# Optimization experiments

Measured on AMD Instinct MI355X. Metric: run time of the kernel, lower is better.

## Reference

```python
import jax, jax.numpy as jnp
import numpy as np

B, L, D, H, E, M, P = 2, 512, 768, 12, 32, 4, 256
EMB, BS, MAP, C = 768, 64, 256, 97


def setup_inputs() -> dict:
    key = jax.random.key(0)
    ks = jax.random.split(key, 16)
    w = lambda k, s: (0.02 * jax.random.normal(k, s, jnp.float32))
    seq = jax.random.normal(ks[0], (B, L, D), jnp.float32)
    attn = jax.random.uniform(ks[1], (B, H, L, L), jnp.float32)
    entity_pos = jax.random.randint(ks[2], (B, E, M), 0, L - 2)
    # distinct (h, t) entity pairs per document -> unique mention-pair scatter slots
    grid = jnp.stack(jnp.meshgrid(jnp.arange(E), jnp.arange(E), indexing='ij'), -1).reshape(-1, 2)
    hts = jnp.stack([grid[jax.random.permutation(jax.random.fold_in(ks[3], b), E * E)[:P]] for b in range(B)], 0)
    mention_idx = jnp.broadcast_to(jnp.arange(E * M).reshape(E, M), (B, E, M))
    return {
        'seq': seq, 'attn': attn,
        'entity_pos': entity_pos, 'hts': hts, 'mention_idx': mention_idx,
        'W_head': w(ks[4], (2 * D, EMB)), 'b_head': jnp.zeros((EMB,), jnp.float32),
        'W_tail': w(ks[5], (2 * D, EMB)), 'b_tail': jnp.zeros((EMB,), jnp.float32),
        'W_rel': w(ks[6], (EMB * BS, C)), 'b_rel': jnp.zeros((C,), jnp.float32),
        'W_fh': w(ks[7], (D, EMB)), 'W_ft': w(ks[8], (D, EMB)), 'b_f': jnp.zeros((EMB,), jnp.float32),
        'W_unet': w(ks[9], (EMB, C)), 'b_unet': jnp.zeros((C,), jnp.float32),
        'W_mlp': w(ks[10], (EMB, C)), 'b_mlp': jnp.zeros((C,), jnp.float32),
        'W_bil': w(ks[11], (3 * C, C)), 'b_bil': jnp.zeros((C,), jnp.float32),
    }


def reference(seq, attn, entity_pos, hts, mention_idx,
              W_head, b_head, W_tail, b_tail, W_rel, b_rel,
              W_fh, W_ft, b_f, W_unet, b_unet, W_mlp, b_mlp, W_bil, b_bil):
    pos = entity_pos + 1                                 # bert offset
    b3 = jnp.arange(B)[:, None, None]
    ment_emb = seq[b3, pos]                              # [B,E,M,D] mention gather
    ment_att = attn[b3, :, pos]                          # [B,E,M,H,L]
    ent_emb = jax.nn.logsumexp(ment_emb, axis=2)         # [B,E,D] logsumexp pool
    ent_att = ment_att.mean(axis=2)                      # [B,E,H,L]
    b2 = jnp.arange(B)[:, None]
    h_idx, t_idx = hts[..., 0], hts[..., 1]
    hs, ts = ent_emb[b2, h_idx], ent_emb[b2, t_idx]      # [B,P,D]
    ha, ta = ent_att[b2, h_idx], ent_att[b2, t_idx]      # [B,P,H,L]
    ht_att = (ha * ta).mean(2)                           # [B,P,L]
    ht_att = ht_att / (ht_att.sum(-1, keepdims=True) + 1e-5)
    rs = jnp.einsum('bld,bpl->bpd', seq, ht_att)         # localized context
    N = B * P
    hz = jnp.tanh(jnp.concatenate([hs, rs], -1).reshape(N, 2 * D) @ W_head + b_head)
    tz = jnp.tanh(jnp.concatenate([ts, rs], -1).reshape(N, 2 * D) @ W_tail + b_tail)
    bl = (hz.reshape(N, EMB // BS, BS, 1) * tz.reshape(N, EMB // BS, 1, BS)).reshape(N, EMB * BS)
    r1 = bl @ W_rel + b_rel                              # [N,C]
    # mention-pair dense map scatter (map_rss)
    ment_flat = ment_emb.reshape(B, E * M, D)
    mh = mention_idx[b2, h_idx]                          # [B,P,M]
    mt = mention_idx[b2, t_idx]
    mh2 = jnp.broadcast_to(mh[:, :, :, None], (B, P, M, M))
    mt2 = jnp.broadcast_to(mt[:, :, None, :], (B, P, M, M))
    b4 = jnp.broadcast_to(jnp.arange(B)[:, None, None, None], (B, P, M, M))
    eh = ment_flat[b4, mh2]                              # [B,P,M,M,D]
    et = ment_flat[b4, mt2]
    feat = eh @ W_fh + et @ W_ft + b_f                   # fused Linear(cat(h,t))
    mp = jnp.zeros((B, MAP, MAP, EMB), seq.dtype).at[b4, mh2, mt2].set(feat)
    enc2 = jnp.tanh(mp @ W_unet + b_unet)                # UNet-channel surrogate
    enc3 = jax.nn.gelu(mp @ W_mlp + b_mlp)               # MLP-channel surrogate
    r2 = jax.nn.logsumexp(enc2[b4, mh2, mt2], axis=(2, 3)).reshape(N, C)
    r3 = jax.nn.logsumexp(enc3[b4, mh2, mt2], axis=(2, 3)).reshape(N, C)
    return jnp.concatenate([r1, r2, r3], -1) @ W_bil + b_bil
```

## Files before the change

kernel.cpp:

```cpp
#include <hip/hip_runtime.h>
#include <hip/hip_bf16.h>

#define B_  2
#define L_  512
#define D_  768
#define H_  12
#define E_  32
#define M_  4
#define P_  256
#define EMB_ 768
#define BS_ 64
#define C_  97
#define N_  (B_*P_)

#define KTOT_    49152
#define CPAD_    112
#define KSPLIT_  48
#define KCHUNK_  (KTOT_/KSPLIT_)
#define PSTR_    128
#define TILE_    (CPAD_*64)

typedef __hip_bfloat16 bf16;
typedef __attribute__((ext_vector_type(8))) short bf16x8;
typedef __attribute__((ext_vector_type(4))) float f32x4;
typedef __attribute__((ext_vector_type(8))) float f32x8;

__device__ inline float ldIn(const void* p, long idx, int isbf) {
    return isbf ? (float)((const bf16*)p)[idx] : ((const float*)p)[idx];
}

__device__ inline unsigned short f2bf(float f) {
    bf16 h = (bf16)f;
    return *(unsigned short*)&h;
}

__device__ inline int detect_bf(const void* seqd) {
    const unsigned short* u = (const unsigned short*)seqd;
    int lane = threadIdx.x & 63;
    unsigned short e = (u[lane] >> 7) & 0xFF;
    unsigned long long m = __ballot(e >= 140);
    return m == 0ull;
}

struct PrepArgs {
    const void* src[8];
    long off[8];
    int K[8];
    int Ncols[8];
    int Npad[8];
    unsigned short* dst[8];
    const void* W_bil;  float* W_bilF;
    const void* b_f; const void* W_unet; const void* b_unet;
    const void* W_mlp; const void* b_mlp; float* c23p;
    const void* W_rel; unsigned short* WBt;
    const void* seqd;
};

union PrepSm {
    float T[32][65];
    unsigned short TW[CPAD_][72];
};

__global__ void prep_kernel(PrepArgs a) {
    int isbf = detect_bf(a.seqd);
    int z = blockIdx.z;
    __shared__ PrepSm sm;
    int tid = threadIdx.x;
    if (z == 0) {
        int lin = blockIdx.y*48 + blockIdx.x;
        if (lin >= 16) return;
        int c = tid;
        if (c >= C_) return;
        float s2 = 0.f, s3 = 0.f;
        int d0 = lin*48;
        for (int i = 0; i < 48; i++) {
            int d = d0 + i;
            float bf = ldIn(a.b_f, d, isbf);
            s2 += bf * ldIn(a.W_unet, (long)d*C_ + c, isbf);
            s3 += bf * ldIn(a.W_mlp,  (long)d*C_ + c, isbf);
        }
        if (lin == 0) {
            s2 += ldIn(a.b_unet, c, isbf);
            s3 += ldIn(a.b_mlp,  c, isbf);
        }
        a.c23p[lin*194 + c]      = s2;
        a.c23p[lin*194 + 97 + c] = s3;
    } else if (z == 1) {
        int lin = blockIdx.y*48 + blockIdx.x;
        if (lin >= KTOT_/64) return;
        int k0 = lin * 64;
        for (int idx = tid; idx < 64*97; idx += 256) {
            int kk = idx / 97, c = idx % 97;
            sm.TW[c][kk] = f2bf(ldIn(a.W_rel, (long)(k0+kk)*C_ + c, isbf));
        }
        for (int idx = tid; idx < 15*64; idx += 256) {
            sm.TW[97 + (idx>>6)][idx & 63] = 0;
        }
        __syncthreads();
        unsigned short* tb = a.WBt + (long)lin*TILE_;
        for (int t = 0; t < 4; t++) {
            int idx = tid + t*256;
            if (idx < 896) {
                int l  = idx & 63;
                int h  = (idx >> 6) & 1;
                int ct = idx >> 7;
                int row = ct*16 + (l & 15);
                int col = h*32 + (l >> 4)*8;
                *(uint4*)(tb + idx*8) = *(uint4*)&sm.TW[row][col];
            }
        }
    } else if (z <= 9) {
        int j = z - 2;
        int K = a.K[j], Ncols = a.Ncols[j], Npad = a.Npad[j];
        int k0 = blockIdx.x*32, n0 = blockIdx.y*64;
        if (k0 >= K || n0 >= Npad) return;
        const void* src = a.src[j];
        long off = a.off[j];
        unsigned short* dst = a.dst[j];
        int r = tid >> 3, c8 = (tid & 7) * 8;
        if ((Ncols & 7) == 0) {
            long base = off + (long)(k0+r)*Ncols + n0 + c8;
            if (isbf) {
                unsigned short tmp[8];
                *(uint4*)tmp = *(const uint4*)((const unsigned short*)src + base);
                #pragma unroll
                for (int e = 0; e < 8; e++) {
                    bf16 hh = *(bf16*)&tmp[e];
                    sm.T[r][c8+e] = (float)hh;
                }
            } else {
                const float* sp = (const float*)src + base;
                float4 x = *(const float4*)sp;
                float4 y = *(const float4*)(sp + 4);
                sm.T[r][c8+0]=x.x; sm.T[r][c8+1]=x.y; sm.T[r][c8+2]=x.z; sm.T[r][c8+3]=x.w;
                sm.T[r][c8+4]=y.x; sm.T[r][c8+5]=y.y; sm.T[r][c8+6]=y.z; sm.T[r][c8+7]=y.w;
            }
        } else {
            #pragma unroll
            for (int e = 0; e < 8; e++) {
                int n = n0 + c8 + e;
                sm.T[r][c8+e] = (n < Ncols) ? ldIn(src, off + (long)(k0+r)*Ncols + n, isbf) : 0.f;
            }
        }
        __syncthreads();
        int nn = tid >> 2, q8 = (tid & 3) * 8;
        unsigned short o[8];
        #pragma unroll
        for (int e = 0; e < 8; e++) o[e] = f2bf(sm.T[q8+e][nn]);
        *(uint4*)(dst + (long)(n0+nn)*K + k0 + q8) = *(uint4*)o;
    } else {
        int lin = blockIdx.y*48 + blockIdx.x;
        int idx = lin*256 + tid;
        if (idx < 291*C_) a.W_bilF[idx] = ldIn(a.W_bil, idx, isbf);
    }
}

__global__ void ghatt_kernel(const void* __restrict__ seq, const void* __restrict__ attn,
                             const int* __restrict__ entity_pos, const int* __restrict__ hts,
                             unsigned short* __restrict__ mentb, float* __restrict__ ent_emb,
                             unsigned short* __restrict__ htb) {
    int isbf = detect_bf(seq);
    if (blockIdx.x < 512) {
        int bp = blockIdx.x;
        int b = bp >> 8;
        int h_e = hts[bp*2+0], t_e = hts[bp*2+1];
        int ph[M_], pt[M_];
        for (int m = 0; m < M_; m++) {
            ph[m] = entity_pos[(b*E_ + h_e)*M_ + m] + 1;
            pt[m] = entity_pos[(b*E_ + t_e)*M_ + m] + 1;
        }
        __shared__ float red[256];
        float v[2];
        for (int t = 0; t < 2; t++) {
            int l = threadIdx.x + t*256;
            float s = 0.f;
            for (int h = 0; h < H_; h++) {
                long hb = ((long)(b*H_ + h))*L_;
                float ha = 0.f, ta = 0.f;
                for (int m = 0; m < M_; m++) {
                    ha += ldIn(attn, (hb + ph[m])*L_ + l, isbf);
                    ta += ldIn(attn, (hb + pt[m])*L_ + l, isbf);
                }
                s += ha * ta;
            }
            v[t] = s * (0.0625f / H_);
        }
        red[threadIdx.x] = v[0] + v[1];
        __syncthreads();
        for (int off = 128; off > 0; off >>= 1) {
            if (threadIdx.x < off) red[threadIdx.x] += red[threadIdx.x+off];
            __syncthreads();
        }
        float inv = 1.0f / (red[0] + 1e-5f);
        for (int t = 0; t < 2; t++) {
            int l = threadIdx.x + t*256;
            htb[(long)bp*L_ + l] = f2bf(v[t] * inv);
        }
    } else {
        int be = blockIdx.x - 512;
        int b = be >> 5;
        int pos[M_];
        for (int m = 0; m < M_; m++) pos[m] = entity_pos[be*M_+m] + 1;
        for (int d = threadIdx.x; d < D_; d += 256) {
            float x[M_];
            for (int m = 0; m < M_; m++) {
                x[m] = ldIn(seq, ((long)b*L_ + pos[m])*D_ + d, isbf);
                mentb[((long)be*M_ + m)*D_ + d] = f2bf(x[m]);
            }
            float mx = fmaxf(fmaxf(x[0],x[1]), fmaxf(x[2],x[3]));
            float s = expf(x[0]-mx)+expf(x[1]-mx)+expf(x[2]-mx)+expf(x[3]-mx);
            ent_emb[(long)be*D_ + d] = mx + logf(s);
        }
    }
}

__global__ void catb_kernel(const float* __restrict__ ent_emb, const float* __restrict__ rs,
                            const int* __restrict__ hts,
                            unsigned short* __restrict__ hcatb, unsigned short* __restrict__ tcatb) {
    int n = blockIdx.x;
    int b = n >> 8;
    int h_e = hts[n*2+0], t_e = hts[n*2+1];
    const float* eh = ent_emb + (long)(b*E_ + h_e)*D_;
    const float* et = ent_emb + (long)(b*E_ + t_e)*D_;
    const float* r  = rs + (long)n*D_;
    for (int k = threadIdx.x; k < D_; k += 256) {
        hcatb[(long)n*1536 + k] = f2bf(eh[k]);
        tcatb[(long)n*1536 + k] = f2bf(et[k]);
        unsigned short rb = f2bf(r[k]);
        hcatb[(long)n*1536 + 768 + k] = rb;
        tcatb[(long)n*1536 + 768 + k] = rb;
    }
}

struct MfmaJob {
    const unsigned short* A[8];
    const unsigned short* Bt[8];
    const void* bias[8];
    void* C[8];
    const void* seqd;
    int K[8];
    int ldc[8];
    int act[8];
    int obf[8];
    int Mt[8];
    int Nt[8];
};

__global__ void mfma_nt2_kernel(MfmaJob args) {
    int z = blockIdx.z;
    int m0 = blockIdx.x*32, n0 = blockIdx.y*32;
    if (m0 >= args.Mt[z] || n0 >= args.Nt[z]) return;
    int isbf = detect_bf(args.seqd);
    const unsigned short* A  = args.A[z];
    const unsigned short* Bt = args.Bt[z];
    const void* bias = args.bias[z];
    void* C = args.C[z];
    int K = args.K[z], ldc = args.ldc[z], act = args.act[z], obf = args.obf[z];
    __shared__ unsigned short Al[2][32][136];
    __shared__ unsigned short Btl[2][32][136];
    int tid = threadIdx.x, wave = tid>>6, lane = tid&63;
    int lm = lane&15, lq = lane>>4;
    int rowg = wave>>1, cgrp = wave&1;
    int rr = tid >> 3;
    int kc = (tid & 7) * 16;
    uint4 ra0, ra1, rb0, rb1;

    ra0 = *(const uint4*)(A  + (long)(m0+rr)*K + kc);
    ra1 = *(const uint4*)(A  + (long)(m0+rr)*K + kc + 8);
    rb0 = *(const uint4*)(Bt + (long)(n0+rr)*K + kc);
    rb1 = *(const uint4*)(Bt + (long)(n0+rr)*K + kc + 8);
    *(uint4*)&Al[0][rr][kc]    = ra0;
    *(uint4*)&Al[0][rr][kc+8]  = ra1;
    *(uint4*)&Btl[0][rr][kc]   = rb0;
    *(uint4*)&Btl[0][rr][kc+8] = rb1;

    int nst = K >> 7;
    f32x4 acc = {};
    for (int ks = 0; ks < nst; ks++) {
        __syncthreads();
        if (ks+1 < nst) {
            int kk = (ks+1) << 7;
            ra0 = *(const uint4*)(A  + (long)(m0+rr)*K + kk + kc);
            ra1 = *(const uint4*)(A  + (long)(m0+rr)*K + kk + kc + 8);
            rb0 = *(const uint4*)(Bt + (long)(n0+rr)*K + kk + kc);
            rb1 = *(const uint4*)(Bt + (long)(n0+rr)*K + kk + kc + 8);
        }
        int cb = ks & 1;
        #pragma unroll
        for (int half = 0; half < 4; half++) {
            bf16x8 af  = *(bf16x8*)&Al[cb][rowg*16+lm][half*32+lq*8];
            bf16x8 bfr = *(bf16x8*)&Btl[cb][cgrp*16+lm][half*32+lq*8];
            acc = __builtin_amdgcn_mfma_f32_16x16x32_bf16(af, bfr, acc, 0, 0, 0);
        }
        if (ks+1 < nst) {
            int nb = (ks+1) & 1;
            *(uint4*)&Al[nb][rr][kc]    = ra0;
            *(uint4*)&Al[nb][rr][kc+8]  = ra1;
            *(uint4*)&Btl[nb][rr][kc]   = rb0;
            *(uint4*)&Btl[nb][rr][kc+8] = rb1;
        }
    }
    int n = n0 + cgrp*16 + lm;
    float bia = bias ? ldIn(bias, n, isbf) : 0.f;
    #pragma unroll
    for (int r = 0; r < 4; r++) {
        int m = m0 + rowg*16 + lq*4 + r;
        float v = acc[r] + bia;
        if (act == 1) v = tanhf(v);
        if (obf) ((unsigned short*)C)[(long)m*ldc + n] = f2bf(v);
        else     ((float*)C)[(long)m*ldc + n] = v;
    }
}

__global__ __launch_bounds__(256, 3)
void r1_mfma_kernel(const float* __restrict__ hz, const float* __restrict__ tz,
                    const unsigned short* __restrict__ WBt,
                    float* __restrict__ partial) {
    __shared__ float hzL[32][17];
    int kz = blockIdx.x;
    int nb0 = blockIdx.y * 32;
    int gk0 = kz * 16;
    int gi0 = kz * 16;
    int g0 = (kz * KCHUNK_) >> 12;
    int tid = threadIdx.x;
    int wave = tid >> 6, lane = tid & 63;
    int lm = lane & 15;
    int ctb = wave * 2;
    int nct = (wave < 3) ? 2 : 1;

    {
        int r = tid >> 3, q = (tid & 7) * 2;
        float2 v = *(const float2*)(hz + (long)(nb0 + r)*EMB_ + gi0 + q);
        hzL[r][q] = v.x; hzL[r][q+1] = v.y;
    }
    int lq = lane >> 4;
    f32x8 tza[2], tzb[2];
    #pragma unroll
    for (int rg = 0; rg < 2; rg++) {
        const float* tp = tz + (long)(nb0 + rg*16 + lm)*EMB_ + g0*64;
        float4 x0 = *(const float4*)(tp + lq*8);
        float4 y0 = *(const float4*)(tp + lq*8 + 4);
        float4 x1 = *(const float4*)(tp + 32 + lq*8);
        float4 y1 = *(const float4*)(tp + 32 + lq*8 + 4);
        tza[rg][0]=x0.x; tza[rg][1]=x0.y; tza[rg][2]=x0.z; tza[rg][3]=x0.w;
        tza[rg][4]=y0.x; tza[rg][5]=y0.y; tza[rg][6]=y0.z; tza[rg][7]=y0.w;
        tzb[rg][0]=x1.x; tzb[rg][1]=x1.y; tzb[rg][2]=x1.z; tzb[rg][3]=x1.w;
        tzb[rg][4]=y1.x; tzb[rg][5]=y1.y; tzb[rg][6]=y1.z; tzb[rg][7]=y1.w;
    }
    __syncthreads();

    const unsigned short* wb = WBt + (long)gk0*TILE_ + lane*8;

    f32x4 acc[2][2] = {};
    bf16x8 cb[2][2];
    #pragma unroll
    for (int ct = 0; ct < 2; ct++)
        if (ct < nct)
            #pragma unroll
            for (int h = 0; h < 2; h++)
                cb[ct][h] = *(const bf16x8*)(wb + ((ctb+ct)*2 + h)*512);

    #pragma unroll 2
    for (int ks = 0; ks < KCHUNK_/64; ks++) {
        bf16x8 nbuf[2][2];
        if (ks+1 < KCHUNK_/64) {
            const unsigned short* wn = wb + (long)(ks+1)*TILE_;
            #pragma unroll
            for (int ct = 0; ct < 2; ct++)
                if (ct < nct)
                    #pragma unroll
                    for (int h = 0; h < 2; h++)
                        nbuf[ct][h] = *(const bf16x8*)(wn + ((ctb+ct)*2 + h)*512);
        }
        float hv0 = hzL[lm][ks];
        float hv1 = hzL[16 + lm][ks];
        unsigned short o00[8], o01[8], o10[8], o11[8];
        #pragma unroll
        for (int e = 0; e < 8; e++) {
            o00[e] = f2bf(tza[0][e] * hv0);
            o01[e] = f2bf(tzb[0][e] * hv0);
            o10[e] = f2bf(tza[1][e] * hv1);
            o11[e] = f2bf(tzb[1][e] * hv1);
        }
        bf16x8 a00 = *(bf16x8*)o00, a01 = *(bf16x8*)o01;
        bf16x8 a10 = *(bf16x8*)o10, a11 = *(bf16x8*)o11;
        #pragma unroll
        for (int ct = 0; ct < 2; ct++) {
            if (ct < nct) {
                acc[ct][0] = __builtin_amdgcn_mfma_f32_16x16x32_bf16(a00, cb[ct][0], acc[ct][0], 0, 0, 0);
                acc[ct][0] = __builtin_amdgcn_mfma_f32_16x16x32_bf16(a01, cb[ct][1], acc[ct][0], 0, 0, 0);
                acc[ct][1] = __builtin_amdgcn_mfma_f32_16x16x32_bf16(a10, cb[ct][0], acc[ct][1], 0, 0, 0);
                acc[ct][1] = __builtin_amdgcn_mfma_f32_16x16x32_bf16(a11, cb[ct][1], acc[ct][1], 0, 0, 0);
            }
        }
        if (ks+1 < KCHUNK_/64) {
            #pragma unroll
            for (int ct = 0; ct < 2; ct++)
                if (ct < nct)
                    #pragma unroll
                    for (int h = 0; h < 2; h++)
                        cb[ct][h] = nbuf[ct][h];
        }
    }
    #pragma unroll
    for (int ct = 0; ct < 2; ct++) {
        if (ct < nct || wave == 3) {
            int c = (ctb + ct)*16 + lm;
            #pragma unroll
            for (int rg = 0; rg < 2; rg++) {
                #pragma unroll
                for (int r = 0; r < 4; r++) {
                    int nl = rg*16 + lq*4 + r;
                    float v = (ct < nct) ? acc[ct][rg][r] : 0.f;
                    partial[((long)(nb0+nl)*KSPLIT_ + kz)*PSTR_ + c] = v;
                }
            }
        }
    }
}

__global__ void r23out_kernel(const float* __restrict__ partial, const void* __restrict__ b_rel,
                              const float* __restrict__ mu, const float* __restrict__ c23p,
                              const int* __restrict__ hts, const int* __restrict__ mention_idx,
                              const float* __restrict__ W_bilF, const void* __restrict__ b_bil,
                              void* __restrict__ out, const void* __restrict__ seqd) {
    int bp = blockIdx.x;
    int b = bp >> 8;
    int c = threadIdx.x;
    int isbf = detect_bf(seqd);
    __shared__ float row[292];
    if (c < C_) {
        const float* pr = partial + (long)bp*KSPLIT_*PSTR_;
        float r1v = 0.f;
        #pragma unroll 8
        for (int kz = 0; kz < KSPLIT_; kz++)
            r1v += pr[kz*PSTR_ + c];
        r1v += ldIn(b_rel, c, isbf);
        int h_e = hts[bp*2+0], t_e = hts[bp*2+1];
        const float* mu2h = mu;
        const float* mu2t = mu + 32768;
        const float* mu3h = mu + 65536;
        const float* mu3t = mu + 98304;
        float ah2[4], at2[4], ah3[4], at3[4];
        for (int m = 0; m < 4; m++) {
            int emh = mention_idx[(b*E_ + h_e)*M_ + m];
            int emt = mention_idx[(b*E_ + t_e)*M_ + m];
            ah2[m] = mu2h[(long)(b*128 + emh)*128 + c];
            ah3[m] = mu3h[(long)(b*128 + emh)*128 + c];
            at2[m] = mu2t[(long)(b*128 + emt)*128 + c];
            at3[m] = mu3t[(long)(b*128 + emt)*128 + c];
        }
        float c2 = 0.f, c3 = 0.f;
        #pragma unroll
        for (int j = 0; j < 16; j++) {
            c2 += c23p[j*194 + c];
            c3 += c23p[j*194 + 97 + c];
        }
        float v2[16], v3[16];
        int q = 0;
        for (int i = 0; i < 4; i++) {
            for (int j = 0; j < 4; j++, q++) {
                float x2 = ah2[i] + at2[j] + c2;
                v2[q] = tanhf(x2);
                float x3 = ah3[i] + at3[j] + c3;
                float t = tanhf(0.7978845608028654f * (x3 + 0.044715f*x3*x3*x3));
                v3[q] = 0.5f * x3 * (1.0f + t);
            }
        }
        float m2 = v2[0], m3 = v3[0];
        for (q = 1; q < 16; q++) { m2 = fmaxf(m2, v2[q]); m3 = fmaxf(m3, v3[q]); }
        float s2 = 0.f, s3 = 0.f;
        for (q = 0; q < 16; q++) { s2 += expf(v2[q]-m2); s3 += expf(v3[q]-m3); }
        row[c]        = r1v;
        row[C_ + c]   = m2 + logf(s2);
        row[2*C_ + c] = m3 + logf(s3);
    }
    __syncthreads();
    if (c >= C_) return;
    float a0 = 0.f, a1 = 0.f, a2 = 0.f, a3 = 0.f;
    #pragma unroll 4
    for (int k = 0; k < 288; k += 4) {
        a0 += row[k+0] * W_bilF[(k+0)*C_ + c];
        a1 += row[k+1] * W_bilF[(k+1)*C_ + c];
        a2 += row[k+2] * W_bilF[(k+2)*C_ + c];
        a3 += row[k+3] * W_bilF[(k+3)*C_ + c];
    }
    a0 += row[288] * W_bilF[288*C_ + c];
    a1 += row[289] * W_bilF[289*C_ + c];
    a2 += row[290] * W_bilF[290*C_ + c];
    float v = a0 + a1 + a2 + a3 + ldIn(b_bil, c, isbf);
    if (isbf) ((bf16*)out)[(long)bp*C_ + c] = (bf16)v;
    else      ((float*)out)[(long)bp*C_ + c] = v;
}

extern "C" void kernel_launch(void* const* d_in, const int* in_sizes, int n_in,
                              void* d_out, int out_size, void* d_ws, size_t ws_size,
                              hipStream_t stream) {
    const void* seq        = d_in[0];
    const void* attn       = d_in[1];
    const int*  entity_pos = (const int*)d_in[2];
    const int*  hts        = (const int*)d_in[3];
    const int*  mention_idx= (const int*)d_in[4];
    const void* W_head     = d_in[5];
    const void* b_head     = d_in[6];
    const void* W_tail     = d_in[7];
    const void* b_tail     = d_in[8];
    const void* W_rel      = d_in[9];
    const void* b_rel      = d_in[10];
    const void* W_fh       = d_in[11];
    const void* W_ft       = d_in[12];
    const void* b_f        = d_in[13];
    const void* W_unet     = d_in[14];
    const void* b_unet     = d_in[15];
    const void* W_mlp      = d_in[16];
    const void* b_mlp      = d_in[17];
    const void* W_bil      = d_in[18];
    const void* b_bil      = d_in[19];

    float* w = (float*)d_ws;
    unsigned short* mentb = (unsigned short*)(w + 64);
    float* ent_emb  = w + 98368;
    unsigned short* htb = (unsigned short*)(w + 540736);
    float* rs       = w + 671808;
    float* hz       = w + 1065024;
    float* tz       = w + 1458240;
    float* mu       = w + 1851456;
    unsigned short* seqT  = (unsigned short*)(w + 1982784);
    unsigned short* WhT   = (unsigned short*)(w + 2376000);
    unsigned short* WtT   = (unsigned short*)(w + 2965824);
    unsigned short* WfhT  = (unsigned short*)(w + 3555648);
    unsigned short* WftT  = (unsigned short*)(w + 3850560);
    unsigned short* WunetT= (unsigned short*)(w + 4145472);
    unsigned short* WmlpT = (unsigned short*)(w + 4194624);
    unsigned short* Tbh   = (unsigned short*)(w + 4243776);
    unsigned short* Tbt   = (unsigned short*)(w + 4342080);
    unsigned short* hcatb = (unsigned short*)(w + 4440384);
    unsigned short* tcatb = (unsigned short*)(w + 4833600);
    unsigned short* WBt   = (unsigned short*)(w + 5226816);
    float* partial  = w + 7979328;
    float* c23p     = w + 11200000;
    float* W_bilF   = w + 11649344;

    {
        PrepArgs a = {};
        const void* srcs[8] = {W_head, W_tail, W_fh, W_ft, W_unet, W_mlp, seq, seq};
        long offs[8]   = {0,0,0,0,0,0,0,393216};
        int Ks[8]      = {1536,1536,768,768,768,768,512,512};
        int Ncols8[8]  = {768,768,768,768,97,97,768,768};
        int Npads[8]   = {768,768,768,768,128,128,768,768};
        unsigned short* dsts[8] = {WhT, WtT, WfhT, WftT, WunetT, WmlpT, seqT, seqT+393216};
        for (int z = 0; z < 8; z++) {
            a.src[z]=srcs[z]; a.off[z]=offs[z]; a.K[z]=Ks[z];
            a.Ncols[z]=Ncols8[z]; a.Npad[z]=Npads[z]; a.dst[z]=dsts[z];
        }
        a.W_bil = W_bil; a.W_bilF = W_bilF;
        a.b_f = b_f; a.W_unet = W_unet; a.b_unet = b_unet;
        a.W_mlp = W_mlp; a.b_mlp = b_mlp; a.c23p = c23p;
        a.W_rel = W_rel; a.WBt = WBt;
        a.seqd = seq;
        prep_kernel<<<dim3(48, 16, 11), 256, 0, stream>>>(a);
    }
    ghatt_kernel<<<512 + 64, 256, 0, stream>>>(seq, attn, entity_pos, hts, mentb, ent_emb, htb);
    {
        MfmaJob ga = {};
        ga.seqd = seq;
        for (int z = 0; z < 2; z++) {
            ga.A[z] = htb + (long)z*256*512; ga.Bt[z] = seqT + (long)z*393216;
            ga.bias[z] = nullptr; ga.C[z] = rs + (long)z*256*768;
            ga.K[z] = 512; ga.ldc[z] = 768; ga.act[z] = 0; ga.obf[z] = 0;
            ga.Mt[z] = 256; ga.Nt[z] = 768;
        }
        ga.A[2] = mentb; ga.Bt[2] = WfhT; ga.bias[2] = nullptr; ga.C[2] = Tbh;
        ga.K[2] = 768; ga.ldc[2] = 768; ga.act[2] = 0; ga.obf[2] = 1;
        ga.Mt[2] = 256; ga.Nt[2] = 768;
        ga.A[3] = mentb; ga.Bt[3] = WftT; ga.bias[3] = nullptr; ga.C[3] = Tbt;
        ga.K[3] = 768; ga.ldc[3] = 768; ga.act[3] = 0; ga.obf[3] = 1;
        ga.Mt[3] = 256; ga.Nt[3] = 768;
        mfma_nt2_kernel<<<dim3(8, 24, 4), 256, 0, stream>>>(ga);
    }
    catb_kernel<<<N_, 256, 0, stream>>>(ent_emb, rs, hts, hcatb, tcatb);
    {
        MfmaJob ga = {};
        ga.seqd = seq;
        ga.A[0] = hcatb; ga.Bt[0] = WhT; ga.bias[0] = b_head; ga.C[0] = hz;
        ga.A[1] = tcatb; ga.Bt[1] = WtT; ga.bias[1] = b_tail; ga.C[1] = tz;
        for (int z = 0; z < 2; z++) {
            ga.K[z] = 1536; ga.ldc[z] = 768; ga.act[z] = 1; ga.obf[z] = 0;
            ga.Mt[z] = 512; ga.Nt[z] = 768;
        }
        const unsigned short* As[4] = {Tbh, Tbt, Tbh, Tbt};
        const unsigned short* Bs[4] = {WunetT, WunetT, WmlpT, WmlpT};
        for (int q = 0; q < 4; q++) {
            int z = 2 + q;
            ga.A[z] = As[q]; ga.Bt[z] = Bs[q]; ga.bias[z] = nullptr;
            ga.C[z] = mu + q*32768;
            ga.K[z] = 768; ga.ldc[z] = 128; ga.act[z] = 0; ga.obf[z] = 0;
            ga.Mt[z] = 256; ga.Nt[z] = 128;
        }
        mfma_nt2_kernel<<<dim3(16, 24, 6), 256, 0, stream>>>(ga);
    }
    r1_mfma_kernel<<<dim3(KSPLIT_, 16), 256, 0, stream>>>(hz, tz, WBt, partial);
    r23out_kernel<<<N_, 128, 0, stream>>>(partial, b_rel, mu, c23p, hts, mention_idx,
                                          W_bilF, b_bil, d_out, seq);
}
```

Baseline: 211.7 us.

## Merge ghatt into prep kernel and gather head/tail inputs inside MFMA GEMM

The ghatt work (attention pair products and mention logsumexp) now runs as an extra z-slice of the prep kernel, removing one launch. The catb kernel is also removed: the head/tail GEMM gathers ent_emb rows by hts, plus the rs rows, directly from fp32 and converts them to bf16 while filling the A tile. This drops one launch and an intermediate bf16 buffer round trip. The cost is an in-loop fp32 load and conversion (twice the A-operand bytes), and the extra prep slice runs as 768 blocks alongside the weight transposes, of which only 576 do work.

Result: no change. 208.1 us (-1.7%).

```diff
diff --git a/kernel.cpp b/kernel.cpp
--- a/kernel.cpp
+++ b/kernel.cpp
@@ -32,6 +32,13 @@
 __device__ inline unsigned short f2bf(float f) {
     bf16 h = (bf16)f;
     return *(unsigned short*)&h;
+}
+
+__device__ inline void cvt16(unsigned short* o, float4 a, float4 b, float4 c, float4 d) {
+    o[0]=f2bf(a.x);  o[1]=f2bf(a.y);  o[2]=f2bf(a.z);  o[3]=f2bf(a.w);
+    o[4]=f2bf(b.x);  o[5]=f2bf(b.y);  o[6]=f2bf(b.z);  o[7]=f2bf(b.w);
+    o[8]=f2bf(c.x);  o[9]=f2bf(c.y);  o[10]=f2bf(c.z); o[11]=f2bf(c.w);
+    o[12]=f2bf(d.x); o[13]=f2bf(d.y); o[14]=f2bf(d.z); o[15]=f2bf(d.w);
 }
 
 __device__ inline int detect_bf(const void* seqd) {
@@ -54,11 +61,14 @@
     const void* W_mlp; const void* b_mlp; float* c23p;
     const void* W_rel; unsigned short* WBt;
     const void* seqd;
+    const void* attn; const int* entity_pos; const int* hts;
+    unsigned short* mentb; float* ent_emb; unsigned short* htb;
 };
 
 union PrepSm {
     float T[32][65];
-    unsigned short TW[CPAD_][72];
+    unsigned short TW[CPAD_][80];
+    float red[256];
 };
 
 __global__ void prep_kernel(PrepArgs a) {
@@ -148,87 +158,64 @@
         #pragma unroll
         for (int e = 0; e < 8; e++) o[e] = f2bf(sm.T[q8+e][nn]);
         *(uint4*)(dst + (long)(n0+nn)*K + k0 + q8) = *(uint4*)o;
-    } else {
+    } else if (z == 10) {
         int lin = blockIdx.y*48 + blockIdx.x;
         int idx = lin*256 + tid;
         if (idx < 291*C_) a.W_bilF[idx] = ldIn(a.W_bil, idx, isbf);
-    }
-}
-
-__global__ void ghatt_kernel(const void* __restrict__ seq, const void* __restrict__ attn,
-                             const int* __restrict__ entity_pos, const int* __restrict__ hts,
-                             unsigned short* __restrict__ mentb, float* __restrict__ ent_emb,
-                             unsigned short* __restrict__ htb) {
-    int isbf = detect_bf(seq);
-    if (blockIdx.x < 512) {
-        int bp = blockIdx.x;
-        int b = bp >> 8;
-        int h_e = hts[bp*2+0], t_e = hts[bp*2+1];
-        int ph[M_], pt[M_];
-        for (int m = 0; m < M_; m++) {
-            ph[m] = entity_pos[(b*E_ + h_e)*M_ + m] + 1;
-            pt[m] = entity_pos[(b*E_ + t_e)*M_ + m] + 1;
-        }
-        __shared__ float red[256];
-        float v[2];
-        for (int t = 0; t < 2; t++) {
-            int l = threadIdx.x + t*256;
-            float s = 0.f;
-            for (int h = 0; h < H_; h++) {
-                long hb = ((long)(b*H_ + h))*L_;
-                float ha = 0.f, ta = 0.f;
+    } else {
+        int lin = blockIdx.y*48 + blockIdx.x;
+        if (lin >= 576) return;
+        if (lin < 512) {
+            int bp = lin;
+            int b = bp >> 8;
+            int h_e = a.hts[bp*2+0], t_e = a.hts[bp*2+1];
+            int ph[M_], pt[M_];
+            for (int m = 0; m < M_; m++) {
+                ph[m] = a.entity_pos[(b*E_ + h_e)*M_ + m] + 1;
+                pt[m] = a.entity_pos[(b*E_ + t_e)*M_ + m] + 1;
+            }
+            float v[2];
+            for (int t = 0; t < 2; t++) {
+                int l = tid + t*256;
+                float s = 0.f;
+                for (int h = 0; h < H_; h++) {
+                    long hb = ((long)(b*H_ + h))*L_;
+                    float ha = 0.f, ta = 0.f;
+                    for (int m = 0; m < M_; m++) {
+                        ha += ldIn(a.attn, (hb + ph[m])*L_ + l, isbf);
+                        ta += ldIn(a.attn, (hb + pt[m])*L_ + l, isbf);
+                    }
+                    s += ha * ta;
+                }
+                v[t] = s * (0.0625f / H_);
+            }
+            sm.red[tid] = v[0] + v[1];
+            __syncthreads();
+            for (int off = 128; off > 0; off >>= 1) {
+                if (tid < off) sm.red[tid] += sm.red[tid+off];
+                __syncthreads();
+            }
+            float inv = 1.0f / (sm.red[0] + 1e-5f);
+            for (int t = 0; t < 2; t++) {
+                int l = tid + t*256;
+                a.htb[(long)bp*L_ + l] = f2bf(v[t] * inv);
+            }
+        } else {
+            int be = lin - 512;
+            int b = be >> 5;
+            int pos[M_];
+            for (int m = 0; m < M_; m++) pos[m] = a.entity_pos[be*M_+m] + 1;
+            for (int d = tid; d < D_; d += 256) {
+                float x[M_];
                 for (int m = 0; m < M_; m++) {
-                    ha += ldIn(attn, (hb + ph[m])*L_ + l, isbf);
-                    ta += ldIn(attn, (hb + pt[m])*L_ + l, isbf);
+                    x[m] = ldIn(a.seqd, ((long)b*L_ + pos[m])*D_ + d, isbf);
+                    a.mentb[((long)be*M_ + m)*D_ + d] = f2bf(x[m]);
                 }
-                s += ha * ta;
-            }
-            v[t] = s * (0.0625f / H_);
-        }
-        red[threadIdx.x] = v[0] + v[1];
-        __syncthreads();
-        for (int off = 128; off > 0; off >>= 1) {
-            if (threadIdx.x < off) red[threadIdx.x] += red[threadIdx.x+off];
-            __syncthreads();
-        }
-        float inv = 1.0f / (red[0] + 1e-5f);
-        for (int t = 0; t < 2; t++) {
-            int l = threadIdx.x + t*256;
-            htb[(long)bp*L_ + l] = f2bf(v[t] * inv);
-        }
-    } else {
-        int be = blockIdx.x - 512;
-        int b = be >> 5;
-        int pos[M_];
-        for (int m = 0; m < M_; m++) pos[m] = entity_pos[be*M_+m] + 1;
-        for (int d = threadIdx.x; d < D_; d += 256) {
-            float x[M_];
-            for (int m = 0; m < M_; m++) {
-                x[m] = ldIn(seq, ((long)b*L_ + pos[m])*D_ + d, isbf);
-                mentb[((long)be*M_ + m)*D_ + d] = f2bf(x[m]);
-            }
-            float mx = fmaxf(fmaxf(x[0],x[1]), fmaxf(x[2],x[3]));
-            float s = expf(x[0]-mx)+expf(x[1]-mx)+expf(x[2]-mx)+expf(x[3]-mx);
-            ent_emb[(long)be*D_ + d] = mx + logf(s);
-        }
-    }
-}
-
-__global__ void catb_kernel(const float* __restrict__ ent_emb, const float* __restrict__ rs,
-                            const int* __restrict__ hts,
-                            unsigned short* __restrict__ hcatb, unsigned short* __restrict__ tcatb) {
-    int n = blockIdx.x;
-    int b = n >> 8;
-    int h_e = hts[n*2+0], t_e = hts[n*2+1];
-    const float* eh = ent_emb + (long)(b*E_ + h_e)*D_;
-    const float* et = ent_emb + (long)(b*E_ + t_e)*D_;
-    const float* r  = rs + (long)n*D_;
-    for (int k = threadIdx.x; k < D_; k += 256) {
-        hcatb[(long)n*1536 + k] = f2bf(eh[k]);
-        tcatb[(long)n*1536 + k] = f2bf(et[k]);
-        unsigned short rb = f2bf(r[k]);
-        hcatb[(long)n*1536 + 768 + k] = rb;
-        tcatb[(long)n*1536 + 768 + k] = rb;
+                float mx = fmaxf(fmaxf(x[0],x[1]), fmaxf(x[2],x[3]));
+                float s = expf(x[0]-mx)+expf(x[1]-mx)+expf(x[2]-mx)+expf(x[3]-mx);
+                a.ent_emb[(long)be*D_ + d] = mx + logf(s);
+            }
+        }
     }
 }
 
@@ -238,12 +225,16 @@
     const void* bias[8];
     void* C[8];
     const void* seqd;
+    const int* hts;
+    const float* ent_emb;
+    const float* rsrc;
     int K[8];
     int ldc[8];
     int act[8];
     int obf[8];
     int Mt[8];
     int Nt[8];
+    int gath[8];
 };
 
 __global__ void mfma_nt2_kernel(MfmaJob args) {
@@ -256,6 +247,7 @@
     const void* bias = args.bias[z];
     void* C = args.C[z];
     int K = args.K[z], ldc = args.ldc[z], act = args.act[z], obf = args.obf[z];
+    int gmode = args.gath[z];
     __shared__ unsigned short Al[2][32][136];
     __shared__ unsigned short Btl[2][32][136];
     int tid = threadIdx.x, wave = tid>>6, lane = tid&63;
@@ -263,14 +255,31 @@
     int rowg = wave>>1, cgrp = wave&1;
     int rr = tid >> 3;
     int kc = (tid & 7) * 16;
+    const float *gh = nullptr, *gr = nullptr;
+    if (gmode) {
+        int m = m0 + rr, b = m >> 8;
+        int ent = args.hts[m*2 + (gmode-1)];
+        gh = args.ent_emb + (long)(b*E_ + ent)*D_ + kc;
+        gr = args.rsrc + (long)m*EMB_ + kc;
+    }
     uint4 ra0, ra1, rb0, rb1;
-
-    ra0 = *(const uint4*)(A  + (long)(m0+rr)*K + kc);
-    ra1 = *(const uint4*)(A  + (long)(m0+rr)*K + kc + 8);
+    float4 fa0, fa1, fa2, fa3;
+
+    if (gmode) {
+        fa0 = *(const float4*)gh;      fa1 = *(const float4*)(gh+4);
+        fa2 = *(const float4*)(gh+8);  fa3 = *(const float4*)(gh+12);
+        unsigned short o[16];
+        cvt16(o, fa0, fa1, fa2, fa3);
+        *(uint4*)&Al[0][rr][kc]   = *(uint4*)o;
+        *(uint4*)&Al[0][rr][kc+8] = *(uint4*)(o+8);
+    } else {
+        ra0 = *(const uint4*)(A + (long)(m0+rr)*K + kc);
+        ra1 = *(const uint4*)(A + (long)(m0+rr)*K + kc + 8);
+        *(uint4*)&Al[0][rr][kc]   = ra0;
+        *(uint4*)&Al[0][rr][kc+8] = ra1;
+    }
     rb0 = *(const uint4*)(Bt + (long)(n0+rr)*K + kc);
     rb1 = *(const uint4*)(Bt + (long)(n0+rr)*K + kc + 8);
-    *(uint4*)&Al[0][rr][kc]    = ra0;
-    *(uint4*)&Al[0][rr][kc+8]  = ra1;
     *(uint4*)&Btl[0][rr][kc]   = rb0;
     *(uint4*)&Btl[0][rr][kc+8] = rb1;
 
@@ -280,8 +289,14 @@
         __syncthreads();
         if (ks+1 < nst) {
             int kk = (ks+1) << 7;
-            ra0 = *(const uint4*)(A  + (long)(m0+rr)*K + kk + kc);
-            ra1 = *(const uint4*)(A  + (long)(m0+rr)*K + kk + kc + 8);
+            if (gmode) {
+                const float* s = (kk < D_) ? (gh + kk) : (gr + kk - D_);
+                fa0 = *(const float4*)s;      fa1 = *(const float4*)(s+4);
+                fa2 = *(const float4*)(s+8);  fa3 = *(const float4*)(s+12);
+            } else {
+                ra0 = *(const uint4*)(A + (long)(m0+rr)*K + kk + kc);
+                ra1 = *(const uint4*)(A + (long)(m0+rr)*K + kk + kc + 8);
+            }
             rb0 = *(const uint4*)(Bt + (long)(n0+rr)*K + kk + kc);
             rb1 = *(const uint4*)(Bt + (long)(n0+rr)*K + kk + kc + 8);
         }
@@ -294,8 +309,15 @@
         }
         if (ks+1 < nst) {
             int nb = (ks+1) & 1;
-            *(uint4*)&Al[nb][rr][kc]    = ra0;
-            *(uint4*)&Al[nb][rr][kc+8]  = ra1;
+            if (gmode) {
+                unsigned short o[16];
+                cvt16(o, fa0, fa1, fa2, fa3);
+                *(uint4*)&Al[nb][rr][kc]   = *(uint4*)o;
+                *(uint4*)&Al[nb][rr][kc+8] = *(uint4*)(o+8);
+            } else {
+                *(uint4*)&Al[nb][rr][kc]   = ra0;
+                *(uint4*)&Al[nb][rr][kc+8] = ra1;
+            }
             *(uint4*)&Btl[nb][rr][kc]   = rb0;
             *(uint4*)&Btl[nb][rr][kc+8] = rb1;
         }
@@ -534,8 +556,6 @@
     unsigned short* WmlpT = (unsigned short*)(w + 4194624);
     unsigned short* Tbh   = (unsigned short*)(w + 4243776);
     unsigned short* Tbt   = (unsigned short*)(w + 4342080);
-    unsigned short* hcatb = (unsigned short*)(w + 4440384);
-    unsigned short* tcatb = (unsigned short*)(w + 4833600);
     unsigned short* WBt   = (unsigned short*)(w + 5226816);
     float* partial  = w + 7979328;
     float* c23p     = w + 11200000;
@@ -558,35 +578,35 @@
         a.W_mlp = W_mlp; a.b_mlp = b_mlp; a.c23p = c23p;
         a.W_rel = W_rel; a.WBt = WBt;
         a.seqd = seq;
-        prep_kernel<<<dim3(48, 16, 11), 256, 0, stream>>>(a);
-    }
-    ghatt_kernel<<<512 + 64, 256, 0, stream>>>(seq, attn, entity_pos, hts, mentb, ent_emb, htb);
+        a.attn = attn; a.entity_pos = entity_pos; a.hts = hts;
+        a.mentb = mentb; a.ent_emb = ent_emb; a.htb = htb;
+        prep_kernel<<<dim3(48, 16, 12), 256, 0, stream>>>(a);
+    }
     {
         MfmaJob ga = {};
-        ga.seqd = seq;
+        ga.seqd = seq; ga.hts = hts; ga.ent_emb = ent_emb; ga.rsrc = rs;
         for (int z = 0; z < 2; z++) {
             ga.A[z] = htb + (long)z*256*512; ga.Bt[z] = seqT + (long)z*393216;
             ga.bias[z] = nullptr; ga.C[z] = rs + (long)z*256*768;
             ga.K[z] = 512; ga.ldc[z] = 768; ga.act[z] = 0; ga.obf[z] = 0;
-            ga.Mt[z] = 256; ga.Nt[z] = 768;
+            ga.Mt[z] = 256; ga.Nt[z] = 768; ga.gath[z] = 0;
         }
         ga.A[2] = mentb; ga.Bt[2] = WfhT; ga.bias[2] = nullptr; ga.C[2] = Tbh;
         ga.K[2] = 768; ga.ldc[2] = 768; ga.act[2] = 0; ga.obf[2] = 1;
-        ga.Mt[2] = 256; ga.Nt[2] = 768;
+        ga.Mt[2] = 256; ga.Nt[2] = 768; ga.gath[2] = 0;
         ga.A[3] = mentb; ga.Bt[3] = WftT; ga.bias[3] = nullptr; ga.C[3] = Tbt;
         ga.K[3] = 768; ga.ldc[3] = 768; ga.act[3] = 0; ga.obf[3] = 1;
-        ga.Mt[3] = 256; ga.Nt[3] = 768;
+        ga.Mt[3] = 256; ga.Nt[3] = 768; ga.gath[3] = 0;
         mfma_nt2_kernel<<<dim3(8, 24, 4), 256, 0, stream>>>(ga);
     }
-    catb_kernel<<<N_, 256, 0, stream>>>(ent_emb, rs, hts, hcatb, tcatb);
     {
         MfmaJob ga = {};
-        ga.seqd = seq;
-        ga.A[0] = hcatb; ga.Bt[0] = WhT; ga.bias[0] = b_head; ga.C[0] = hz;
-        ga.A[1] = tcatb; ga.Bt[1] = WtT; ga.bias[1] = b_tail; ga.C[1] = tz;
+        ga.seqd = seq; ga.hts = hts; ga.ent_emb = ent_emb; ga.rsrc = rs;
+        ga.A[0] = nullptr; ga.Bt[0] = WhT; ga.bias[0] = b_head; ga.C[0] = hz;
+        ga.A[1] = nullptr; ga.Bt[1] = WtT; ga.bias[1] = b_tail; ga.C[1] = tz;
         for (int z = 0; z < 2; z++) {
             ga.K[z] = 1536; ga.ldc[z] = 768; ga.act[z] = 1; ga.obf[z] = 0;
-            ga.Mt[z] = 512; ga.Nt[z] = 768;
+            ga.Mt[z] = 512; ga.Nt[z] = 768; ga.gath[z] = z + 1;
         }
         const unsigned short* As[4] = {Tbh, Tbt, Tbh, Tbt};
         const unsigned short* Bs[4] = {WunetT, WunetT, WmlpT, WmlpT};
@@ -595,7 +615,7 @@
             ga.A[z] = As[q]; ga.Bt[z] = Bs[q]; ga.bias[z] = nullptr;
             ga.C[z] = mu + q*32768;
             ga.K[z] = 768; ga.ldc[z] = 128; ga.act[z] = 0; ga.obf[z] = 0;
-            ga.Mt[z] = 256; ga.Nt[z] = 128;
+            ga.Mt[z] = 256; ga.Nt[z] = 128; ga.gath[z] = 0;
         }
         mfma_nt2_kernel<<<dim3(16, 24, 6), 256, 0, stream>>>(ga);
     }
```
